# Performance work log

Measured on AMD Instinct MI355X. Metric: run time of the kernel, lower is better.

The kernel has to match this reference:

```python
import jax, jax.numpy as jnp
import numpy as np

BLOCK = 8
SCALE = 0.5  # deterministic choice from scale_factors=[0.5, 0.75]


def setup_inputs() -> dict:
    key = jax.random.key(0)
    k1, k2 = jax.random.split(key)
    B, C, H, W = 32, 3, 512, 512
    x = jax.random.uniform(k1, (B, C, H, W), dtype=jnp.float32) * 2.0 - 1.0  # images in [-1,1]
    # per-8x8-block uniform values u in [0,1); noise = (u - 0.5)/50
    block_noise = jax.random.uniform(k2, (B, H // BLOCK, W // BLOCK), dtype=jnp.float32)
    return {"x": x, "block_noise": block_noise}


def reference(x, block_noise):
    B, C, H, W = x.shape
    nH, nW = int(H * SCALE), int(W * SCALE)
    # bilinear down then up, half-pixel centers == torch align_corners=False
    x_ds = jax.image.resize(x, (B, C, nH, nW), method="bilinear")
    x_rec = jax.image.resize(x_ds, (B, C, H, W), method="bilinear")
    # block noise: one scalar per 8x8 block, broadcast over channels
    noise = (block_noise - 0.5) / 50.0  # [B, H/8, W/8]
    noise_full = jnp.repeat(jnp.repeat(noise, BLOCK, axis=1), BLOCK, axis=2)  # [B, H, W]
    out = jnp.clip(x_rec + noise_full[:, None, :, :], -1.0, 1.0)
    return out
```

## Files before the change

### kernel.cpp

```cpp
#include <hip/hip_runtime.h>


typedef float f32x4 __attribute__((ext_vector_type(4)));

namespace {
constexpr int IMG = 512;
constexpr int TY = 16;
constexpr int HROWS = TY + 6;
constexpr float I32 = 1.0f / 32.0f;
constexpr float I7  = 1.0f / 7.0f;
constexpr float I28 = 1.0f / 28.0f;
}

__device__ __forceinline__ f32x4 vfma(float w, f32x4 a, f32x4 acc) {
  acc.x = fmaf(w, a.x, acc.x); acc.y = fmaf(w, a.y, acc.y);
  acc.z = fmaf(w, a.z, acc.z); acc.w = fmaf(w, a.w, acc.w);
  return acc;
}
__device__ __forceinline__ f32x4 vmul(float w, f32x4 a) {
  f32x4 r; r.x = w * a.x; r.y = w * a.y; r.z = w * a.z; r.w = w * a.w;
  return r;
}

__global__ __launch_bounds__(1024, 8) void compress_fused7_kernel(
    const float* __restrict__ x, const float* __restrict__ bn,
    float* __restrict__ out) {
  const int nwg = gridDim.x;
  const int cpx = nwg >> 3;
  const int bid = blockIdx.x;
  const int logical = (bid & 7) * cpx + (bid >> 3);
  const int ty = logical & 31;
  const int plane = logical >> 5;
  const int b = plane / 3;
  const int y0 = ty * TY;
  const int tid = threadIdx.x;
  const int cg = tid & 127;
  const int rs = tid >> 7;
  const int gx0 = 4 * cg;

  __shared__ float H[HROWS][IMG];

  const float* xp = x + (size_t)plane * (IMG * IMG);
  float* op = out + (size_t)plane * (IMG * IMG);

  const float nzv =
      (bn[(size_t)b * 4096 + ((y0 + 2 * rs) >> 3) * 64 + (cg >> 1)] - 0.5f) * 0.02f;

  const bool left  = (cg == 0);
  const bool right = (cg == 127);
  const int A0 = left ? 0 : (right ? IMG - 12 : gx0 - 4);

  auto rowptr = [&](int r) -> const f32x4* {
    int g = y0 - 3 + r;
    g = max(0, min(IMG - 1, g));
    return (const f32x4*)(xp + (size_t)g * IMG + A0);
  };

  auto hconv = [&](f32x4 qa, f32x4 qb, f32x4 qc) -> f32x4 {
    const float f0 = qa.x, f1 = qa.y, f2 = qa.z, f3 = qa.w;
    const float f4_ = qb.x, f5 = qb.y, f6 = qb.z, f7 = qb.w;
    const float f8 = qc.x, f9 = qc.y, f10 = qc.z, f11 = qc.w;
    f32x4 h;
    if (left) {
      h.x = (3.f * f0 + 3.f * f1 + f2) * I7;
      h.y = 9*I28*f0 + (9*I28 + I32)*f1 + (3*I28 + 3*I32)*f2 + 3*I32*f3 + I32*f4_;
      h.z = 3*I28*f0 + (3*I28 + 3*I32)*f1 + (I28 + 9*I32)*f2 + 9*I32*f3 + 3*I32*f4_;
      h.w = (3.f*f1 + 9.f*f2 + 10.f*f3 + 6.f*f4_ + 3.f*f5 + f6) * I32;
    } else if (right) {
      h.x = (f5 + 3.f*f6 + 6.f*f7 + 10.f*f8 + 9.f*f9 + 3.f*f10) * I32;
      h.y = 3*I32*f7 + 9*I32*f8 + (I28 + 9*I32)*f9 + (3*I28 + 3*I32)*f10 + 3*I28*f11;
      h.z = I32*f7 + 3*I32*f8 + (3*I28 + 3*I32)*f9 + (9*I28 + I32)*f10 + 9*I28*f11;
      h.w = (f9 + 3.f*f10 + 3.f*f11) * I7;
    } else {
      h.x = (f1 + 3.f*f2 + 6.f*f3 + 10.f*f4_ + 9.f*f5 + 3.f*f6) * I32;
      h.y = (3.f*f3 + 9.f*f4_ + 10.f*f5 + 6.f*f6 + 3.f*f7 + f8) * I32;
      h.z = (f3 + 3.f*f4_ + 6.f*f5 + 10.f*f6 + 9.f*f7 + 3.f*f8) * I32;
      h.w = (3.f*f5 + 9.f*f6 + 10.f*f7 + 6.f*f8 + 3.f*f9 + f10) * I32;
    }
    return h;
  };

  const bool has2 = (rs < 6);
  const f32x4* p0 = rowptr(rs);
  const f32x4* p1 = rowptr(rs + 8);
  f32x4 a0 = p0[0], b0 = p0[1], c0 = p0[2];
  f32x4 a1 = p1[0], b1 = p1[1], c1 = p1[2];

  *(f32x4*)&H[rs][gx0] = hconv(a0, b0, c0);

  f32x4 a2, b2, c2;
  if (has2) { const f32x4* p2 = rowptr(rs + 16); a2 = p2[0]; b2 = p2[1]; c2 = p2[2]; }

  *(f32x4*)&H[rs + 8][gx0] = hconv(a1, b1, c1);
  if (has2) *(f32x4*)&H[rs + 16][gx0] = hconv(a2, b2, c2);
  __syncthreads();

  const int wb = 2 * rs;
  const bool top = (y0 == 0);
  const bool bot = (y0 == IMG - TY);
  const int gy0 = y0 + 2 * rs;

#define LDQ(j) (*(const f32x4*)&H[wb + (j)][gx0])
  const f32x4 q0 = LDQ(0), q1 = LDQ(1), q2 = LDQ(2), q3 = LDQ(3);
  const f32x4 q4 = LDQ(4), q5 = LDQ(5), q6 = LDQ(6), q7 = LDQ(7);
#undef LDQ

  f32x4 oE, oO;
  if (top && rs == 0) {
    oE = vfma(3*I7, q3, vfma(3*I7, q4, vmul(I7, q5)));
    oO = vfma(9*I28, q3, vfma(9*I28 + I32, q4,
         vfma(3*I28 + 3*I32, q5, vfma(3*I32, q6, vmul(I32, q7)))));
  } else if (top && rs == 1) {
    oE = vfma(3*I28, q1, vfma(3*I28 + 3*I32, q2,
         vfma(I28 + 9*I32, q3, vfma(9*I32, q4, vmul(3*I32, q5)))));
    oO = vfma(3*I32, q2, vfma(9*I32, q3, vfma(10*I32, q4,
         vfma(6*I32, q5, vfma(3*I32, q6, vmul(I32, q7))))));
  } else if (bot && rs == 6) {
    oE = vfma(I32, q0, vfma(3*I32, q1, vfma(6*I32, q2,
         vfma(10*I32, q3, vfma(9*I32, q4, vmul(3*I32, q5))))));
    oO = vfma(3*I32, q2, vfma(9*I32, q3, vfma(I28 + 9*I32, q4,
         vfma(3*I28 + 3*I32, q5, vmul(3*I28, q6)))));
  } else if (bot && rs == 7) {
    oE = vfma(I32, q0, vfma(3*I32, q1, vfma(3*I28 + 3*I32, q2,
         vfma(9*I28 + I32, q3, vmul(9*I28, q4)))));
    oO = vfma(I7, q2, vfma(3*I7, q3, vmul(3*I7, q4)));
  } else {
    oE = vfma(I32, q0, vfma(3*I32, q1, vfma(6*I32, q2,
         vfma(10*I32, q3, vfma(9*I32, q4, vmul(3*I32, q5))))));
    oO = vfma(3*I32, q2, vfma(9*I32, q3, vfma(10*I32, q4,
         vfma(6*I32, q5, vfma(3*I32, q6, vmul(I32, q7))))));
  }

#define FINISH_STORE(o, ii)                                                    \
  {                                                                            \
    f32x4 v = o;                                                               \
    v.x = fminf(1.f, fmaxf(-1.f, v.x + nzv));                                  \
    v.y = fminf(1.f, fmaxf(-1.f, v.y + nzv));                                  \
    v.z = fminf(1.f, fmaxf(-1.f, v.z + nzv));                                  \
    v.w = fminf(1.f, fmaxf(-1.f, v.w + nzv));                                  \
    __builtin_nontemporal_store(v, (f32x4*)(op + (size_t)(gy0 + ii) * IMG + gx0)); \
  }
  FINISH_STORE(oE, 0)
  FINISH_STORE(oO, 1)
#undef FINISH_STORE
}

extern "C" void kernel_launch(void* const* d_in, const int* in_sizes, int n_in,
                              void* d_out, int out_size, void* d_ws, size_t ws_size,
                              hipStream_t stream) {
  const float* x  = (const float*)d_in[0];
  const float* bn = (const float*)d_in[1];
  float* out = (float*)d_out;

  const int n_planes = in_sizes[0] / (IMG * IMG);
  const int nwg = (IMG / TY) * n_planes;
  compress_fused7_kernel<<<dim3(nwg), dim3(1024), 0, stream>>>(x, bn, out);
}
```

Baseline: 38.31 us.

## Replace shared-memory row staging with per-thread register vertical convolution over 4 rows

Drops the LDS tile and __syncthreads: each thread now loads 10 clamped input rows, does the horizontal conv in registers, and accumulates the vertical taps directly into 4 output rows. Blocks shrink to 512 threads covering 16 rows. This removes LDS traffic and the barrier, but each thread now recomputes overlapping horizontal convs (10 rows for 4 outputs versus about 22 for 16 before), so global loads and ALU work per output go up.

```diff
diff --git a/kernel.cpp b/kernel.cpp
--- a/kernel.cpp
+++ b/kernel.cpp
@@ -5,8 +5,6 @@
 
 namespace {
 constexpr int IMG = 512;
-constexpr int TY = 16;
-constexpr int HROWS = TY + 6;
 constexpr float I32 = 1.0f / 32.0f;
 constexpr float I7  = 1.0f / 7.0f;
 constexpr float I28 = 1.0f / 28.0f;
@@ -17,41 +15,36 @@
   acc.z = fmaf(w, a.z, acc.z); acc.w = fmaf(w, a.w, acc.w);
   return acc;
 }
-__device__ __forceinline__ f32x4 vmul(float w, f32x4 a) {
-  f32x4 r; r.x = w * a.x; r.y = w * a.y; r.z = w * a.z; r.w = w * a.w;
-  return r;
-}
 
-__global__ __launch_bounds__(1024, 8) void compress_fused7_kernel(
+__global__ __launch_bounds__(512, 8) void compress_fused8_kernel(
     const float* __restrict__ x, const float* __restrict__ bn,
     float* __restrict__ out) {
   const int nwg = gridDim.x;
   const int cpx = nwg >> 3;
   const int bid = blockIdx.x;
   const int logical = (bid & 7) * cpx + (bid >> 3);
-  const int ty = logical & 31;
+  const int tg = logical & 31;
   const int plane = logical >> 5;
   const int b = plane / 3;
-  const int y0 = ty * TY;
   const int tid = threadIdx.x;
   const int cg = tid & 127;
-  const int rs = tid >> 7;
+  const int qs = tid >> 7;
+  const int q  = tg * 4 + qs;
+  const int gy0 = 4 * q;
   const int gx0 = 4 * cg;
-
-  __shared__ float H[HROWS][IMG];
 
   const float* xp = x + (size_t)plane * (IMG * IMG);
   float* op = out + (size_t)plane * (IMG * IMG);
 
   const float nzv =
-      (bn[(size_t)b * 4096 + ((y0 + 2 * rs) >> 3) * 64 + (cg >> 1)] - 0.5f) * 0.02f;
+      (bn[(size_t)b * 4096 + (q >> 1) * 64 + (cg >> 1)] - 0.5f) * 0.02f;
 
   const bool left  = (cg == 0);
   const bool right = (cg == 127);
   const int A0 = left ? 0 : (right ? IMG - 12 : gx0 - 4);
 
-  auto rowptr = [&](int r) -> const f32x4* {
-    int g = y0 - 3 + r;
+  auto rowp = [&](int j) -> const f32x4* {
+    int g = gy0 - 3 + j;
     g = max(0, min(IMG - 1, g));
     return (const f32x4*)(xp + (size_t)g * IMG + A0);
   };
@@ -80,56 +73,81 @@
     return h;
   };
 
-  const bool has2 = (rs < 6);
-  const f32x4* p0 = rowptr(rs);
-  const f32x4* p1 = rowptr(rs + 8);
-  f32x4 a0 = p0[0], b0 = p0[1], c0 = p0[2];
-  f32x4 a1 = p1[0], b1 = p1[1], c1 = p1[2];
+  f32x4 acc0 = {0.f,0.f,0.f,0.f}, acc1 = acc0, acc2 = acc0, acc3 = acc0;
+  const int kind = (q == 0) ? 1 : ((q == 127) ? 2 : 0);
 
-  *(f32x4*)&H[rs][gx0] = hconv(a0, b0, c0);
+#define STEP(J, H)                                                             \
+  if (kind == 0) {                                                             \
+    if ((J) == 0) { acc0 = vfma(1*I32, H, acc0); }                             \
+    if ((J) == 1) { acc0 = vfma(3*I32, H, acc0); }                             \
+    if ((J) == 2) { acc0 = vfma(6*I32, H, acc0); acc1 = vfma(3*I32, H, acc1);  \
+                    acc2 = vfma(1*I32, H, acc2); }                             \
+    if ((J) == 3) { acc0 = vfma(10*I32, H, acc0); acc1 = vfma(9*I32, H, acc1); \
+                    acc2 = vfma(3*I32, H, acc2); }                             \
+    if ((J) == 4) { acc0 = vfma(9*I32, H, acc0); acc1 = vfma(10*I32, H, acc1); \
+                    acc2 = vfma(6*I32, H, acc2); acc3 = vfma(3*I32, H, acc3); }\
+    if ((J) == 5) { acc0 = vfma(3*I32, H, acc0); acc1 = vfma(6*I32, H, acc1);  \
+                    acc2 = vfma(10*I32, H, acc2); acc3 = vfma(9*I32, H, acc3);}\
+    if ((J) == 6) { acc1 = vfma(3*I32, H, acc1); acc2 = vfma(9*I32, H, acc2);  \
+                    acc3 = vfma(10*I32, H, acc3); }                            \
+    if ((J) == 7) { acc1 = vfma(1*I32, H, acc1); acc2 = vfma(3*I32, H, acc2);  \
+                    acc3 = vfma(6*I32, H, acc3); }                             \
+    if ((J) == 8) { acc3 = vfma(3*I32, H, acc3); }                             \
+    if ((J) == 9) { acc3 = vfma(1*I32, H, acc3); }                             \
+  } else if (kind == 1) {               \
+    if ((J) == 3) { acc0 = vfma(3*I7, H, acc0); acc1 = vfma(9*I28, H, acc1);   \
+                    acc2 = vfma(3*I28, H, acc2); }                             \
+    if ((J) == 4) { acc0 = vfma(3*I7, H, acc0);                                \
+                    acc1 = vfma(9*I28 + I32, H, acc1);                         \
+                    acc2 = vfma(3*I28 + 3*I32, H, acc2);                       \
+                    acc3 = vfma(3*I32, H, acc3); }                             \
+    if ((J) == 5) { acc0 = vfma(I7, H, acc0);                                  \
+                    acc1 = vfma(3*I28 + 3*I32, H, acc1);                       \
+                    acc2 = vfma(I28 + 9*I32, H, acc2);                         \
+                    acc3 = vfma(9*I32, H, acc3); }                             \
+    if ((J) == 6) { acc1 = vfma(3*I32, H, acc1); acc2 = vfma(9*I32, H, acc2);  \
+                    acc3 = vfma(10*I32, H, acc3); }                            \
+    if ((J) == 7) { acc1 = vfma(I32, H, acc1); acc2 = vfma(3*I32, H, acc2);    \
+                    acc3 = vfma(6*I32, H, acc3); }                             \
+    if ((J) == 8) { acc3 = vfma(3*I32, H, acc3); }                             \
+    if ((J) == 9) { acc3 = vfma(I32, H, acc3); }                               \
+  } else {         \
+    if ((J) == 0) { acc0 = vfma(1*I32, H, acc0); }                             \
+    if ((J) == 1) { acc0 = vfma(3*I32, H, acc0); }                             \
+    if ((J) == 2) { acc0 = vfma(6*I32, H, acc0); acc1 = vfma(3*I32, H, acc1);  \
+                    acc2 = vfma(1*I32, H, acc2); }                             \
+    if ((J) == 3) { acc0 = vfma(10*I32, H, acc0); acc1 = vfma(9*I32, H, acc1); \
+                    acc2 = vfma(3*I32, H, acc2); }                             \
+    if ((J) == 4) { acc0 = vfma(9*I32, H, acc0);                               \
+                    acc1 = vfma(I28 + 9*I32, H, acc1);                         \
+                    acc2 = vfma(3*I28 + 3*I32, H, acc2);                       \
+                    acc3 = vfma(I7, H, acc3); }                                \
+    if ((J) == 5) { acc0 = vfma(3*I32, H, acc0);                               \
+                    acc1 = vfma(3*I28 + 3*I32, H, acc1);                       \
+                    acc2 = vfma(9*I28 + I32, H, acc2);                         \
+                    acc3 = vfma(3*I7, H, acc3); }                              \
+    if ((J) == 6) { acc1 = vfma(3*I28, H, acc1); acc2 = vfma(9*I28, H, acc2);  \
+                    acc3 = vfma(3*I7, H, acc3); }                              \
+  }
 
-  f32x4 a2, b2, c2;
-  if (has2) { const f32x4* p2 = rowptr(rs + 16); a2 = p2[0]; b2 = p2[1]; c2 = p2[2]; }
+#define LOADR(J, A, B, C) { const f32x4* p = rowp(J); A = p[0]; B = p[1]; C = p[2]; }
 
-  *(f32x4*)&H[rs + 8][gx0] = hconv(a1, b1, c1);
-  if (has2) *(f32x4*)&H[rs + 16][gx0] = hconv(a2, b2, c2);
-  __syncthreads();
-
-  const int wb = 2 * rs;
-  const bool top = (y0 == 0);
-  const bool bot = (y0 == IMG - TY);
-  const int gy0 = y0 + 2 * rs;
-
-#define LDQ(j) (*(const f32x4*)&H[wb + (j)][gx0])
-  const f32x4 q0 = LDQ(0), q1 = LDQ(1), q2 = LDQ(2), q3 = LDQ(3);
-  const f32x4 q4 = LDQ(4), q5 = LDQ(5), q6 = LDQ(6), q7 = LDQ(7);
-#undef LDQ
-
-  f32x4 oE, oO;
-  if (top && rs == 0) {
-    oE = vfma(3*I7, q3, vfma(3*I7, q4, vmul(I7, q5)));
-    oO = vfma(9*I28, q3, vfma(9*I28 + I32, q4,
-         vfma(3*I28 + 3*I32, q5, vfma(3*I32, q6, vmul(I32, q7)))));
-  } else if (top && rs == 1) {
-    oE = vfma(3*I28, q1, vfma(3*I28 + 3*I32, q2,
-         vfma(I28 + 9*I32, q3, vfma(9*I32, q4, vmul(3*I32, q5)))));
-    oO = vfma(3*I32, q2, vfma(9*I32, q3, vfma(10*I32, q4,
-         vfma(6*I32, q5, vfma(3*I32, q6, vmul(I32, q7))))));
-  } else if (bot && rs == 6) {
-    oE = vfma(I32, q0, vfma(3*I32, q1, vfma(6*I32, q2,
-         vfma(10*I32, q3, vfma(9*I32, q4, vmul(3*I32, q5))))));
-    oO = vfma(3*I32, q2, vfma(9*I32, q3, vfma(I28 + 9*I32, q4,
-         vfma(3*I28 + 3*I32, q5, vmul(3*I28, q6)))));
-  } else if (bot && rs == 7) {
-    oE = vfma(I32, q0, vfma(3*I32, q1, vfma(3*I28 + 3*I32, q2,
-         vfma(9*I28 + I32, q3, vmul(9*I28, q4)))));
-    oO = vfma(I7, q2, vfma(3*I7, q3, vmul(3*I7, q4)));
-  } else {
-    oE = vfma(I32, q0, vfma(3*I32, q1, vfma(6*I32, q2,
-         vfma(10*I32, q3, vfma(9*I32, q4, vmul(3*I32, q5))))));
-    oO = vfma(3*I32, q2, vfma(9*I32, q3, vfma(10*I32, q4,
-         vfma(6*I32, q5, vfma(3*I32, q6, vmul(I32, q7))))));
-  }
+  f32x4 A0v, B0v, C0v, A1v, B1v, C1v, A2v, B2v, C2v, h;
+  LOADR(0, A0v, B0v, C0v)
+  LOADR(1, A1v, B1v, C1v)
+  LOADR(2, A2v, B2v, C2v)
+  h = hconv(A0v, B0v, C0v); STEP(0, h) LOADR(3, A0v, B0v, C0v)
+  h = hconv(A1v, B1v, C1v); STEP(1, h) LOADR(4, A1v, B1v, C1v)
+  h = hconv(A2v, B2v, C2v); STEP(2, h) LOADR(5, A2v, B2v, C2v)
+  h = hconv(A0v, B0v, C0v); STEP(3, h) LOADR(6, A0v, B0v, C0v)
+  h = hconv(A1v, B1v, C1v); STEP(4, h) LOADR(7, A1v, B1v, C1v)
+  h = hconv(A2v, B2v, C2v); STEP(5, h) LOADR(8, A2v, B2v, C2v)
+  h = hconv(A0v, B0v, C0v); STEP(6, h) LOADR(9, A0v, B0v, C0v)
+  h = hconv(A1v, B1v, C1v); STEP(7, h)
+  h = hconv(A2v, B2v, C2v); STEP(8, h)
+  h = hconv(A0v, B0v, C0v); STEP(9, h)
+#undef LOADR
+#undef STEP
 
 #define FINISH_STORE(o, ii)                                                    \
   {                                                                            \
@@ -140,8 +158,10 @@
     v.w = fminf(1.f, fmaxf(-1.f, v.w + nzv));                                  \
     __builtin_nontemporal_store(v, (f32x4*)(op + (size_t)(gy0 + ii) * IMG + gx0)); \
   }
-  FINISH_STORE(oE, 0)
-  FINISH_STORE(oO, 1)
+  FINISH_STORE(acc0, 0)
+  FINISH_STORE(acc1, 1)
+  FINISH_STORE(acc2, 2)
+  FINISH_STORE(acc3, 3)
 #undef FINISH_STORE
 }
 
@@ -153,6 +173,6 @@
   float* out = (float*)d_out;
 
   const int n_planes = in_sizes[0] / (IMG * IMG);
-  const int nwg = (IMG / TY) * n_planes;
-  compress_fused7_kernel<<<dim3(nwg), dim3(1024), 0, stream>>>(x, bn, out);
+  const int nwg = 32 * n_planes;
+  compress_fused8_kernel<<<dim3(nwg), dim3(512), 0, stream>>>(x, bn, out);
 }
```

Result: slower. 90.34 us (+135.8%).
